# Performance work log

Hardware: AMD Instinct MI355X
Metric: run time of the kernel (lower is better)

The kernel has to match this reference:

```python
import jax, jax.numpy as jnp
import numpy as np

D_MODEL = 256
NHEAD = 8
HEAD_DIM = D_MODEL // NHEAD
CLIP = 10.0
LN_EPS = 1e-5


def setup_inputs() -> dict:
    key = jax.random.key(0)
    ks = jax.random.split(key, 10)
    B, N, d = 2, 256, D_MODEL
    s = 1.0 / np.sqrt(d)
    return {
        "nodes": jax.random.normal(ks[0], (B, N, d), jnp.float32),
        "edges": jax.random.normal(ks[1], (B, N, N, d), jnp.float32),
        # shared projection (used for Q, K, V, edge-Q, edge-K, output)
        "W": jax.random.normal(ks[2], (d, d), jnp.float32) * s,
        "b": jax.random.normal(ks[3], (d,), jnp.float32) * 0.01,
        # shared LayerNorm params (same module applied twice)
        "ln_g": jnp.ones((d,), jnp.float32),
        "ln_b": jnp.zeros((d,), jnp.float32),
        # feedforward
        "W1": jax.random.normal(ks[4], (d, 4 * d), jnp.float32) * s,
        "b1": jnp.zeros((4 * d,), jnp.float32),
        "W2": jax.random.normal(ks[5], (4 * d, d), jnp.float32) * (1.0 / np.sqrt(4 * d)),
        "b2": jnp.zeros((d,), jnp.float32),
    }


def _layer_norm(x, g, b):
    mu = jnp.mean(x, axis=-1, keepdims=True)
    var = jnp.var(x, axis=-1, keepdims=True)
    return (x - mu) * jax.lax.rsqrt(var + LN_EPS) * g + b


def reference(nodes, edges, W, b, ln_g, ln_b, W1, b1, W2, b2):
    B, N, d = nodes.shape
    h, hd = NHEAD, HEAD_DIM

    x = _layer_norm(nodes, ln_g, ln_b)

    # Node projections (shared weight -> q == k == v)
    nq = (x @ W + b).reshape(B, N, h, hd)
    nk = nq
    nv = nq

    # Edge projections (shared weight -> eq == ek)
    eq = (edges @ W + b).reshape(B, N, N, h, hd)
    ek = eq

    # Broadcast-add node+edge queries/keys: [B, N, N, h, hd]
    query = eq + nq[:, :, None, :, :]
    key = ek + nk[:, None, :, :, :]

    scores = jnp.einsum("bijhd,bijhd->bhij", query, key) / np.sqrt(hd)
    scores = CLIP * jnp.tanh(scores)
    attn = jax.nn.softmax(scores, axis=-1)  # [B, h, N, N]

    # attn @ V: [B, h, N, hd] -> [B, N, d]
    out = jnp.einsum("bhij,bjhd->bihd", attn, nv).reshape(B, N, d)
    out = out @ W + b

    x = x + out
    x = _layer_norm(x, ln_g, ln_b)
    ff = jax.nn.gelu(x @ W1 + b1, approximate=False) @ W2 + b2
    return ff + x
```

## Files before the change

### kernel.cpp

```cpp
#include <hip/hip_runtime.h>

typedef _Float16 half_t;
typedef __attribute__((ext_vector_type(8))) _Float16 f16x8;
typedef __attribute__((ext_vector_type(4))) float f32x4;

#define DM 256
#define NH 8
#define HD 32
#define NN 256
#define NB 2
#define JT 32
#define KC 64

__global__ __launch_bounds__(256) void k_ln(const float* __restrict__ in,
                                            const float* __restrict__ g,
                                            const float* __restrict__ be,
                                            float* __restrict__ out) {
  int row = blockIdx.x, t = threadIdx.x;
  float v = in[(size_t)row * DM + t];
  float s = v, q = v * v;
#pragma unroll
  for (int m = 1; m <= 32; m <<= 1) {
    s += __shfl_xor(s, m, 64);
    q += __shfl_xor(q, m, 64);
  }
  __shared__ float as_[4], aq_[4];
  int w = t >> 6, l = t & 63;
  if (l == 0) { as_[w] = s; aq_[w] = q; }
  __syncthreads();
  s = as_[0] + as_[1] + as_[2] + as_[3];
  q = aq_[0] + aq_[1] + aq_[2] + aq_[3];
  float mu = s * (1.0f / DM);
  float var = q * (1.0f / DM) - mu * mu;
  out[(size_t)row * DM + t] = (v - mu) * rsqrtf(var + 1e-5f) * g[t] + be[t];
}

__global__ __launch_bounds__(256) void k_wt16(const float* __restrict__ W,
                                              half_t* __restrict__ WT) {
  int c = blockIdx.x, t = threadIdx.x;
  WT[c * DM + t] = (half_t)W[t * DM + c];
}

template <int K, bool RES>
__global__ __launch_bounds__(1024) void k_gemm(const float* __restrict__ X,
                                               const float* __restrict__ W,
                                               const float* __restrict__ bias,
                                               const float* __restrict__ res,
                                               float* __restrict__ out) {
  __shared__ float sx[8 * K];
  const int t = threadIdx.x;
  const int r0 = blockIdx.x * 8;
  for (int u = t; u < 2 * K; u += 1024) {
    int row = u / (K / 4), c4 = u % (K / 4);
    ((f32x4*)sx)[u] = *(const f32x4*)(X + (size_t)(r0 + row) * K + c4 * 4);
  }
  __syncthreads();
  const int col = t & 255;
  const int rg = t >> 8;
  const float* x0 = sx + (rg * 2) * K;
  const float* x1 = sx + (rg * 2 + 1) * K;
  float a0 = 0.f, a1 = 0.f;
#pragma unroll 8
  for (int k = 0; k < K; ++k) {
    float wv = W[(size_t)k * 256 + col];
    a0 += x0[k] * wv;
    a1 += x1[k] * wv;
  }
  float bb = bias[col];
  a0 += bb; a1 += bb;
  size_t o0 = (size_t)(r0 + rg * 2) * 256 + col;
  size_t o1 = o0 + 256;
  if (RES) { a0 += res[o0]; a1 += res[o1]; }
  out[o0] = a0;
  out[o1] = a1;
}

__global__ __launch_bounds__(1024) void k_ffn1(const float* __restrict__ ys,
                                               const float* __restrict__ W1,
                                               const float* __restrict__ b1,
                                               float* __restrict__ g) {
  __shared__ float sx[8 * DM];
  const int t = threadIdx.x;
  const int r0 = blockIdx.x * 8;
  if (t < 512) {
    int row = t >> 6, c4 = t & 63;
    ((f32x4*)sx)[t] = *(const f32x4*)(ys + (size_t)(r0 + row) * DM + c4 * 4);
  }
  __syncthreads();
  float acc[8];
  float bb = b1[t];
#pragma unroll
  for (int r = 0; r < 8; ++r) acc[r] = bb;
#pragma unroll 8
  for (int k = 0; k < DM; ++k) {
    float wv = W1[(size_t)k * 1024 + t];
#pragma unroll
    for (int r = 0; r < 8; ++r) acc[r] += sx[r * DM + k] * wv;
  }
#pragma unroll
  for (int r = 0; r < 8; ++r) {
    float v = acc[r];
    g[(size_t)(r0 + r) * 1024 + t] = 0.5f * v * (1.0f + erff(v * 0.70710678118654752f));
  }
}

__global__ __launch_bounds__(256, 3) void k_edge_scores(
    const float* __restrict__ edges, const half_t* __restrict__ WT,
    const float* __restrict__ xs, const float* __restrict__ bias,
    float* __restrict__ scores) {
  __shared__ __align__(16) char smem[40960];
  const int tid = threadIdx.x;
  const int l = tid & 63;
  const int w = tid >> 6;
  const int idx = blockIdx.x;
  const int jb = idx & 7;
  const int i = (idx >> 3) & (NN - 1);
  const int b = idx >> 11;
  const int j0 = jb * JT;

  f32x4 accq[4][2], acck[4][2];
#pragma unroll
  for (int ct = 0; ct < 4; ++ct) {
    f32x4 bv = *(const f32x4*)(bias + w * 64 + ct * 16 + (l >> 4) * 4);
    f32x4 iv = {2.f * bv[0], 2.f * bv[1], 2.f * bv[2], 2.f * bv[3]};
#pragma unroll
    for (int jt = 0; jt < 2; ++jt) { accq[ct][jt] = iv; acck[ct][jt] = iv; }
  }

  const float* eg = edges + ((size_t)(b * NN + i) * NN + j0) * DM;
  const float* xb = xs + (size_t)b * NN * DM;
  const float* xi = xb + (size_t)i * DM;
  const int f4 = tid & 15, row0 = tid >> 4;

  f32x4 pe[2], pxj[2], pxi;
#pragma unroll
  for (int q = 0; q < 2; ++q) {
    int row = row0 + q * 16;
    pe[q] = *(const f32x4*)(eg + row * DM + f4 * 4);
    pxj[q] = *(const f32x4*)(xb + (size_t)(j0 + row) * DM + f4 * 4);
  }
  pxi = *(const f32x4*)(xi + f4 * 4);

  for (int kc = 0; kc < 4; ++kc) {
    {
      const char* wtb = (const char*)WT;
#pragma unroll
      for (int q = 0; q < 8; ++q) {
        int ub = (w * 8 + q) * 64;
        int cc = (ub + l) >> 3;
        int ss = l & 7;
        const void* src = wtb + cc * 512 + kc * 128 + ((ss ^ (cc & 7)) * 16);
        __builtin_amdgcn_global_load_lds(
            (const __attribute__((address_space(1))) unsigned int*)src,
            (__attribute__((address_space(3))) unsigned int*)(smem + 8192 + ub * 16),
            16, 0, 0);
      }
    }
#pragma unroll
    for (int q = 0; q < 2; ++q) {
      int row = row0 + q * 16;
      union { unsigned long long u; half_t h[4]; } a1, a2;
#pragma unroll
      for (int z = 0; z < 4; ++z) {
        a1.h[z] = (half_t)(pe[q][z] + pxi[z]);
        a2.h[z] = (half_t)(pe[q][z] + pxj[q][z]);
      }
      int off = (row * 128 + f4 * 8) ^ ((row & 7) << 4);
      *(unsigned long long*)(smem + off) = a1.u;
      *(unsigned long long*)(smem + 4096 + off) = a2.u;
    }
    __syncthreads();
    if (kc < 3) {
#pragma unroll
      for (int q = 0; q < 2; ++q) {
        int row = row0 + q * 16;
        pe[q] = *(const f32x4*)(eg + row * DM + (kc + 1) * KC + f4 * 4);
        pxj[q] = *(const f32x4*)(xb + (size_t)(j0 + row) * DM + (kc + 1) * KC + f4 * 4);
      }
      pxi = *(const f32x4*)(xi + (kc + 1) * KC + f4 * 4);
    }
#pragma unroll
    for (int ks = 0; ks < 2; ++ks) {
      f16x8 fq[2], fk[2];
#pragma unroll
      for (int jt = 0; jt < 2; ++jt) {
        int r = jt * 16 + (l & 15);
        int off = (r * 128 + ks * 64 + ((l >> 4) * 16)) ^ ((r & 7) << 4);
        fq[jt] = *(const f16x8*)(smem + off);
        fk[jt] = *(const f16x8*)(smem + 4096 + off);
      }
#pragma unroll
      for (int ct = 0; ct < 4; ++ct) {
        int c = w * 64 + ct * 16 + (l & 15);
        int off = (c * 128 + ks * 64 + ((l >> 4) * 16)) ^ ((c & 7) << 4);
        f16x8 wf = *(const f16x8*)(smem + 8192 + off);
#pragma unroll
        for (int jt = 0; jt < 2; ++jt) {
          accq[ct][jt] = __builtin_amdgcn_mfma_f32_16x16x32_f16(wf, fq[jt], accq[ct][jt], 0, 0, 0);
          acck[ct][jt] = __builtin_amdgcn_mfma_f32_16x16x32_f16(wf, fk[jt], acck[ct][jt], 0, 0, 0);
        }
      }
    }
    __syncthreads();
  }

  const float scale = 0.17677669529663687f;
#pragma unroll
  for (int a = 0; a < 2; ++a) {
#pragma unroll
    for (int jt = 0; jt < 2; ++jt) {
      float s = 0.f;
#pragma unroll
      for (int u = 0; u < 2; ++u) {
        int ct = a * 2 + u;
#pragma unroll
        for (int rr = 0; rr < 4; ++rr) s += accq[ct][jt][rr] * acck[ct][jt][rr];
      }
      s += __shfl_xor(s, 16, 64);
      s += __shfl_xor(s, 32, 64);
      float sc = 10.0f * tanhf(s * scale);
      if (l < 16) {
        int h = w * 2 + a;
        int jg = j0 + jt * 16 + l;
        scores[(((size_t)(b * NH) + h) * NN + i) * NN + jg] = sc;
      }
    }
  }
}

__global__ __launch_bounds__(1024) void k_smax_av(const float* __restrict__ scores,
                                                  const float* __restrict__ nqv,
                                                  float* __restrict__ ao) {
  __shared__ float sp[NH * NN];
  __shared__ float pp[4 * 256];
  const int t = threadIdx.x;
  const int b = blockIdx.x >> 8, i = blockIdx.x & 255;
#pragma unroll
  for (int p = 0; p < 2; ++p) {
    int idx = p * 1024 + t;
    sp[idx] = scores[(((size_t)(b * NH) + (idx >> 8)) * NN + i) * NN + (idx & 255)];
  }
  __syncthreads();
  const int w = t >> 6, l = t & 63;
  if (w < 8) {
    f32x4 v = *(f32x4*)(sp + w * NN + l * 4);
    float m = fmaxf(fmaxf(v[0], v[1]), fmaxf(v[2], v[3]));
#pragma unroll
    for (int mm = 1; mm <= 32; mm <<= 1) m = fmaxf(m, __shfl_xor(m, mm, 64));
    v[0] = __expf(v[0] - m); v[1] = __expf(v[1] - m);
    v[2] = __expf(v[2] - m); v[3] = __expf(v[3] - m);
    float s = v[0] + v[1] + v[2] + v[3];
#pragma unroll
    for (int mm = 1; mm <= 32; mm <<= 1) s += __shfl_xor(s, mm, 64);
    float inv = 1.0f / s;
    v[0] *= inv; v[1] *= inv; v[2] *= inv; v[3] *= inv;
    *(f32x4*)(sp + w * NN + l * 4) = v;
  }
  __syncthreads();
  const int d = t & 255, jg = t >> 8, h = d >> 5;
  const float* vb = nqv + (size_t)b * NN * DM;
  float acc = 0.f;
#pragma unroll 8
  for (int jj = 0; jj < 64; ++jj) {
    int j = jg * 64 + jj;
    acc += sp[h * 256 + j] * vb[(size_t)j * DM + d];
  }
  pp[jg * 256 + d] = acc;
  __syncthreads();
  if (t < 256)
    ao[((size_t)(b * NN) + i) * DM + t] = pp[t] + pp[256 + t] + pp[512 + t] + pp[768 + t];
}

extern "C" void kernel_launch(void* const* d_in, const int* in_sizes, int n_in,
                              void* d_out, int out_size, void* d_ws, size_t ws_size,
                              hipStream_t stream) {
  const float* nodes = (const float*)d_in[0];
  const float* edges = (const float*)d_in[1];
  const float* W     = (const float*)d_in[2];
  const float* bias  = (const float*)d_in[3];
  const float* ln_g  = (const float*)d_in[4];
  const float* ln_b  = (const float*)d_in[5];
  const float* W1    = (const float*)d_in[6];
  const float* b1    = (const float*)d_in[7];
  const float* W2    = (const float*)d_in[8];
  const float* b2    = (const float*)d_in[9];
  float* out = (float*)d_out;

  char* ws = (char*)d_ws;
  float*  xs     = (float*)(ws + 0x000000);
  float*  nqv    = (float*)(ws + 0x080000);
  half_t* WT16   = (half_t*)(ws + 0x100000);
  float*  scores = (float*)(ws + 0x120000);
  float*  g      = (float*)(ws + 0x120000);
  float*  ao     = (float*)(ws + 0x520000);
  float*  ysr    = (float*)(ws + 0x5A0000);
  float*  ys     = (float*)(ws + 0x620000);

  k_ln<<<NB * NN, 256, 0, stream>>>(nodes, ln_g, ln_b, xs);
  k_wt16<<<DM, 256, 0, stream>>>(W, WT16);
  k_gemm<256, false><<<NB * NN / 8, 1024, 0, stream>>>(xs, W, bias, nullptr, nqv);
  k_edge_scores<<<NB * NN * (NN / JT), 256, 0, stream>>>(edges, WT16, xs, bias, scores);
  k_smax_av<<<NB * NN, 1024, 0, stream>>>(scores, nqv, ao);
  k_gemm<256, true><<<NB * NN / 8, 1024, 0, stream>>>(ao, W, bias, xs, ysr);
  k_ln<<<NB * NN, 256, 0, stream>>>(ysr, ln_g, ln_b, ys);
  k_ffn1<<<NB * NN / 8, 1024, 0, stream>>>(ys, W1, b1, g);
  k_gemm<1024, true><<<NB * NN / 8, 1024, 0, stream>>>(g, W2, b2, ys, out);
}
```

Before: 380.5 us.

## Fuse LN with projections, split-K small GEMMs, load edge weights directly to registers

LayerNorm is fused into the node projection, and the output projection is fused with the residual add and the second LayerNorm, which removes two launches. The small GEMMs now process 2 rows per block with split-K partial sums reduced in shared memory, giving 256 blocks instead of 64 for more parallelism. In the edge-score kernel, W fragments are read from global memory (L2) straight into registers instead of being staged through LDS, which cuts LDS use from 40KB to 8KB for higher occupancy. The cost is repeated global weight reads per wave.

```diff
diff --git a/kernel.cpp b/kernel.cpp
--- a/kernel.cpp
+++ b/kernel.cpp
@@ -6,33 +6,60 @@
 
 #define DM 256
 #define NH 8
-#define HD 32
 #define NN 256
 #define NB 2
 #define JT 32
 #define KC 64
 
-__global__ __launch_bounds__(256) void k_ln(const float* __restrict__ in,
-                                            const float* __restrict__ g,
-                                            const float* __restrict__ be,
-                                            float* __restrict__ out) {
-  int row = blockIdx.x, t = threadIdx.x;
-  float v = in[(size_t)row * DM + t];
+__global__ __launch_bounds__(1024) void k_ln_proj(
+    const float* __restrict__ nodes, const float* __restrict__ W,
+    const float* __restrict__ bias, const float* __restrict__ ln_g,
+    const float* __restrict__ ln_b, float* __restrict__ xs,
+    float* __restrict__ nqv) {
+  __shared__ float sx[2][DM];
+  __shared__ float pp[4][2][DM];
+  __shared__ float rs[8], rq[8];
+  const int t = threadIdx.x;
+  const int r0 = blockIdx.x * 2;
+  const int row = t >> 8, col = t & 255;
+  float v = 0.f;
+  if (t < 512) v = nodes[(size_t)(r0 + row) * DM + col];
   float s = v, q = v * v;
 #pragma unroll
   for (int m = 1; m <= 32; m <<= 1) {
     s += __shfl_xor(s, m, 64);
     q += __shfl_xor(q, m, 64);
   }
-  __shared__ float as_[4], aq_[4];
-  int w = t >> 6, l = t & 63;
-  if (l == 0) { as_[w] = s; aq_[w] = q; }
-  __syncthreads();
-  s = as_[0] + as_[1] + as_[2] + as_[3];
-  q = aq_[0] + aq_[1] + aq_[2] + aq_[3];
-  float mu = s * (1.0f / DM);
-  float var = q * (1.0f / DM) - mu * mu;
-  out[(size_t)row * DM + t] = (v - mu) * rsqrtf(var + 1e-5f) * g[t] + be[t];
+  if (t < 512 && (t & 63) == 0) { rs[t >> 6] = s; rq[t >> 6] = q; }
+  __syncthreads();
+  if (t < 512) {
+    int rb = row * 4;
+    float ss = rs[rb] + rs[rb + 1] + rs[rb + 2] + rs[rb + 3];
+    float qq = rq[rb] + rq[rb + 1] + rq[rb + 2] + rq[rb + 3];
+    float mu = ss * (1.f / DM);
+    float var = qq * (1.f / DM) - mu * mu;
+    float xv = (v - mu) * rsqrtf(var + 1e-5f) * ln_g[col] + ln_b[col];
+    sx[row][col] = xv;
+    xs[(size_t)(r0 + row) * DM + col] = xv;
+  }
+  __syncthreads();
+  const int rg = t >> 8;
+  float a0 = 0.f, a1 = 0.f;
+#pragma unroll 8
+  for (int kk = 0; kk < 64; ++kk) {
+    int k = rg * 64 + kk;
+    float wv = W[(size_t)k * DM + col];
+    a0 += sx[0][k] * wv;
+    a1 += sx[1][k] * wv;
+  }
+  pp[rg][0][col] = a0;
+  pp[rg][1][col] = a1;
+  __syncthreads();
+  if (t < 512) {
+    float r = pp[0][row][col] + pp[1][row][col] + pp[2][row][col] +
+              pp[3][row][col] + bias[col];
+    nqv[(size_t)(r0 + row) * DM + col] = r;
+  }
 }
 
 __global__ __launch_bounds__(256) void k_wt16(const float* __restrict__ W,
@@ -41,74 +68,11 @@
   WT[c * DM + t] = (half_t)W[t * DM + c];
 }
 
-template <int K, bool RES>
-__global__ __launch_bounds__(1024) void k_gemm(const float* __restrict__ X,
-                                               const float* __restrict__ W,
-                                               const float* __restrict__ bias,
-                                               const float* __restrict__ res,
-                                               float* __restrict__ out) {
-  __shared__ float sx[8 * K];
-  const int t = threadIdx.x;
-  const int r0 = blockIdx.x * 8;
-  for (int u = t; u < 2 * K; u += 1024) {
-    int row = u / (K / 4), c4 = u % (K / 4);
-    ((f32x4*)sx)[u] = *(const f32x4*)(X + (size_t)(r0 + row) * K + c4 * 4);
-  }
-  __syncthreads();
-  const int col = t & 255;
-  const int rg = t >> 8;
-  const float* x0 = sx + (rg * 2) * K;
-  const float* x1 = sx + (rg * 2 + 1) * K;
-  float a0 = 0.f, a1 = 0.f;
-#pragma unroll 8
-  for (int k = 0; k < K; ++k) {
-    float wv = W[(size_t)k * 256 + col];
-    a0 += x0[k] * wv;
-    a1 += x1[k] * wv;
-  }
-  float bb = bias[col];
-  a0 += bb; a1 += bb;
-  size_t o0 = (size_t)(r0 + rg * 2) * 256 + col;
-  size_t o1 = o0 + 256;
-  if (RES) { a0 += res[o0]; a1 += res[o1]; }
-  out[o0] = a0;
-  out[o1] = a1;
-}
-
-__global__ __launch_bounds__(1024) void k_ffn1(const float* __restrict__ ys,
-                                               const float* __restrict__ W1,
-                                               const float* __restrict__ b1,
-                                               float* __restrict__ g) {
-  __shared__ float sx[8 * DM];
-  const int t = threadIdx.x;
-  const int r0 = blockIdx.x * 8;
-  if (t < 512) {
-    int row = t >> 6, c4 = t & 63;
-    ((f32x4*)sx)[t] = *(const f32x4*)(ys + (size_t)(r0 + row) * DM + c4 * 4);
-  }
-  __syncthreads();
-  float acc[8];
-  float bb = b1[t];
-#pragma unroll
-  for (int r = 0; r < 8; ++r) acc[r] = bb;
-#pragma unroll 8
-  for (int k = 0; k < DM; ++k) {
-    float wv = W1[(size_t)k * 1024 + t];
-#pragma unroll
-    for (int r = 0; r < 8; ++r) acc[r] += sx[r * DM + k] * wv;
-  }
-#pragma unroll
-  for (int r = 0; r < 8; ++r) {
-    float v = acc[r];
-    g[(size_t)(r0 + r) * 1024 + t] = 0.5f * v * (1.0f + erff(v * 0.70710678118654752f));
-  }
-}
-
 __global__ __launch_bounds__(256, 3) void k_edge_scores(
     const float* __restrict__ edges, const half_t* __restrict__ WT,
     const float* __restrict__ xs, const float* __restrict__ bias,
     float* __restrict__ scores) {
-  __shared__ __align__(16) char smem[40960];
+  __shared__ __align__(16) char smem[8192];
   const int tid = threadIdx.x;
   const int l = tid & 63;
   const int w = tid >> 6;
@@ -131,6 +95,7 @@
   const float* xb = xs + (size_t)b * NN * DM;
   const float* xi = xb + (size_t)i * DM;
   const int f4 = tid & 15, row0 = tid >> 4;
+  const char* wtb = (const char*)WT;
 
   f32x4 pe[2], pxj[2], pxi;
 #pragma unroll
@@ -142,20 +107,15 @@
   pxi = *(const f32x4*)(xi + f4 * 4);
 
   for (int kc = 0; kc < 4; ++kc) {
-    {
-      const char* wtb = (const char*)WT;
-#pragma unroll
-      for (int q = 0; q < 8; ++q) {
-        int ub = (w * 8 + q) * 64;
-        int cc = (ub + l) >> 3;
-        int ss = l & 7;
-        const void* src = wtb + cc * 512 + kc * 128 + ((ss ^ (cc & 7)) * 16);
-        __builtin_amdgcn_global_load_lds(
-            (const __attribute__((address_space(1))) unsigned int*)src,
-            (__attribute__((address_space(3))) unsigned int*)(smem + 8192 + ub * 16),
-            16, 0, 0);
-      }
-    }
+    f16x8 wf[2][4];
+#pragma unroll
+    for (int ks = 0; ks < 2; ++ks)
+#pragma unroll
+      for (int ct = 0; ct < 4; ++ct) {
+        int c = w * 64 + ct * 16 + (l & 15);
+        wf[ks][ct] = *(const f16x8*)(wtb + c * 512 + kc * 128 + ks * 64 +
+                                     ((l >> 4) * 16));
+      }
 #pragma unroll
     for (int q = 0; q < 2; ++q) {
       int row = row0 + q * 16;
@@ -190,16 +150,12 @@
         fk[jt] = *(const f16x8*)(smem + 4096 + off);
       }
 #pragma unroll
-      for (int ct = 0; ct < 4; ++ct) {
-        int c = w * 64 + ct * 16 + (l & 15);
-        int off = (c * 128 + ks * 64 + ((l >> 4) * 16)) ^ ((c & 7) << 4);
-        f16x8 wf = *(const f16x8*)(smem + 8192 + off);
+      for (int ct = 0; ct < 4; ++ct)
 #pragma unroll
         for (int jt = 0; jt < 2; ++jt) {
-          accq[ct][jt] = __builtin_amdgcn_mfma_f32_16x16x32_f16(wf, fq[jt], accq[ct][jt], 0, 0, 0);
-          acck[ct][jt] = __builtin_amdgcn_mfma_f32_16x16x32_f16(wf, fk[jt], acck[ct][jt], 0, 0, 0);
+          accq[ct][jt] = __builtin_amdgcn_mfma_f32_16x16x32_f16(wf[ks][ct], fq[jt], accq[ct][jt], 0, 0, 0);
+          acck[ct][jt] = __builtin_amdgcn_mfma_f32_16x16x32_f16(wf[ks][ct], fk[jt], acck[ct][jt], 0, 0, 0);
         }
-      }
     }
     __syncthreads();
   }
@@ -269,6 +225,106 @@
   __syncthreads();
   if (t < 256)
     ao[((size_t)(b * NN) + i) * DM + t] = pp[t] + pp[256 + t] + pp[512 + t] + pp[768 + t];
+}
+
+__global__ __launch_bounds__(1024) void k_gemm_res_ln(
+    const float* __restrict__ ao, const float* __restrict__ W,
+    const float* __restrict__ bias, const float* __restrict__ xs,
+    const float* __restrict__ ln_g, const float* __restrict__ ln_b,
+    float* __restrict__ ys) {
+  __shared__ float sa[2][DM];
+  __shared__ float pp[4][2][DM];
+  __shared__ float rs[8], rq[8];
+  const int t = threadIdx.x;
+  const int r0 = blockIdx.x * 2;
+  const int row = t >> 8, col = t & 255;
+  if (t < 512) sa[row][col] = ao[(size_t)(r0 + row) * DM + col];
+  __syncthreads();
+  const int rg = t >> 8;
+  float a0 = 0.f, a1 = 0.f;
+#pragma unroll 8
+  for (int kk = 0; kk < 64; ++kk) {
+    int k = rg * 64 + kk;
+    float wv = W[(size_t)k * DM + col];
+    a0 += sa[0][k] * wv;
+    a1 += sa[1][k] * wv;
+  }
+  pp[rg][0][col] = a0;
+  pp[rg][1][col] = a1;
+  __syncthreads();
+  float val = 0.f;
+  if (t < 512) {
+    val = pp[0][row][col] + pp[1][row][col] + pp[2][row][col] +
+          pp[3][row][col] + bias[col] + xs[(size_t)(r0 + row) * DM + col];
+  }
+  float s = val, q = val * val;
+#pragma unroll
+  for (int m = 1; m <= 32; m <<= 1) {
+    s += __shfl_xor(s, m, 64);
+    q += __shfl_xor(q, m, 64);
+  }
+  if (t < 512 && (t & 63) == 0) { rs[t >> 6] = s; rq[t >> 6] = q; }
+  __syncthreads();
+  if (t < 512) {
+    int rb = row * 4;
+    float ss = rs[rb] + rs[rb + 1] + rs[rb + 2] + rs[rb + 3];
+    float qq = rq[rb] + rq[rb + 1] + rq[rb + 2] + rq[rb + 3];
+    float mu = ss * (1.f / DM);
+    float var = qq * (1.f / DM) - mu * mu;
+    ys[(size_t)(r0 + row) * DM + col] =
+        (val - mu) * rsqrtf(var + 1e-5f) * ln_g[col] + ln_b[col];
+  }
+}
+
+__global__ __launch_bounds__(1024) void k_ffn1(const float* __restrict__ ys,
+                                               const float* __restrict__ W1,
+                                               const float* __restrict__ b1,
+                                               float* __restrict__ g) {
+  __shared__ float sy[2][DM];
+  const int t = threadIdx.x;
+  const int r0 = blockIdx.x * 2;
+  if (t < 512) sy[t >> 8][t & 255] = ys[(size_t)(r0 + (t >> 8)) * DM + (t & 255)];
+  __syncthreads();
+  float a0 = b1[t], a1 = a0;
+#pragma unroll 8
+  for (int k = 0; k < DM; ++k) {
+    float wv = W1[(size_t)k * 1024 + t];
+    a0 += sy[0][k] * wv;
+    a1 += sy[1][k] * wv;
+  }
+  g[(size_t)r0 * 1024 + t] = 0.5f * a0 * (1.0f + erff(a0 * 0.70710678118654752f));
+  g[(size_t)(r0 + 1) * 1024 + t] = 0.5f * a1 * (1.0f + erff(a1 * 0.70710678118654752f));
+}
+
+__global__ __launch_bounds__(1024) void k_ffn2(const float* __restrict__ g,
+                                               const float* __restrict__ W2,
+                                               const float* __restrict__ b2,
+                                               const float* __restrict__ ys,
+                                               float* __restrict__ out) {
+  __shared__ float sg[2][1024];
+  __shared__ float pp[4][2][256];
+  const int t = threadIdx.x;
+  const int r0 = blockIdx.x * 2;
+  if (t < 512) ((f32x4*)sg)[t] = *(const f32x4*)(g + (size_t)r0 * 1024 + t * 4);
+  __syncthreads();
+  const int kg = t >> 8, col = t & 255;
+  float a0 = 0.f, a1 = 0.f;
+#pragma unroll 8
+  for (int kk = 0; kk < 256; ++kk) {
+    int k = kg * 256 + kk;
+    float wv = W2[(size_t)k * 256 + col];
+    a0 += sg[0][k] * wv;
+    a1 += sg[1][k] * wv;
+  }
+  pp[kg][0][col] = a0;
+  pp[kg][1][col] = a1;
+  __syncthreads();
+  if (t < 512) {
+    int row = t >> 8;
+    float r = pp[0][row][col] + pp[1][row][col] + pp[2][row][col] +
+              pp[3][row][col] + b2[col] + ys[(size_t)(r0 + row) * DM + col];
+    out[(size_t)(r0 + row) * DM + col] = r;
+  }
 }
 
 extern "C" void kernel_launch(void* const* d_in, const int* in_sizes, int n_in,
@@ -293,16 +349,13 @@
   float*  scores = (float*)(ws + 0x120000);
   float*  g      = (float*)(ws + 0x120000);
   float*  ao     = (float*)(ws + 0x520000);
-  float*  ysr    = (float*)(ws + 0x5A0000);
-  float*  ys     = (float*)(ws + 0x620000);
-
-  k_ln<<<NB * NN, 256, 0, stream>>>(nodes, ln_g, ln_b, xs);
+  float*  ys     = (float*)(ws + 0x5A0000);
+
+  k_ln_proj<<<NB * NN / 2, 1024, 0, stream>>>(nodes, W, bias, ln_g, ln_b, xs, nqv);
   k_wt16<<<DM, 256, 0, stream>>>(W, WT16);
-  k_gemm<256, false><<<NB * NN / 8, 1024, 0, stream>>>(xs, W, bias, nullptr, nqv);
   k_edge_scores<<<NB * NN * (NN / JT), 256, 0, stream>>>(edges, WT16, xs, bias, scores);
   k_smax_av<<<NB * NN, 1024, 0, stream>>>(scores, nqv, ao);
-  k_gemm<256, true><<<NB * NN / 8, 1024, 0, stream>>>(ao, W, bias, xs, ysr);
-  k_ln<<<NB * NN, 256, 0, stream>>>(ysr, ln_g, ln_b, ys);
-  k_ffn1<<<NB * NN / 8, 1024, 0, stream>>>(ys, W1, b1, g);
-  k_gemm<1024, true><<<NB * NN / 8, 1024, 0, stream>>>(g, W2, b2, ys, out);
-}
+  k_gemm_res_ln<<<NB * NN / 2, 1024, 0, stream>>>(ao, W, bias, xs, ln_g, ln_b, ys);
+  k_ffn1<<<NB * NN / 2, 1024, 0, stream>>>(ys, W1, b1, g);
+  k_ffn2<<<NB * NN / 2, 1024, 0, stream>>>(g, W2, b2, ys, out);
+}
```

Measured after the change: 319.2 us. -16.1%, faster.
